# Kernel optimization log

Measured on AMD Instinct MI355X. Metric: run time of the kernel, lower is better.

The kernel has to match this reference:

```python
import jax, jax.numpy as jnp
import numpy as np

B, T, C, H = 8, 1024, 1024, 8
D = C // H  # head dim

def setup_inputs() -> dict:
    key = jax.random.key(0)
    ks = jax.random.split(key, 6)
    s = 1.0 / np.sqrt(C)
    return {
        "x": jax.random.normal(ks[0], (B, T, C), jnp.float32),
        "mask": jnp.ones((B, T), jnp.int32),
        "Wq": jax.random.normal(ks[1], (C, C), jnp.float32) * s,
        "bq": jnp.zeros((C,), jnp.float32),
        "Wk": jax.random.normal(ks[2], (C, C), jnp.float32) * s,
        "bk": jnp.zeros((C,), jnp.float32),
        "Wv": jax.random.normal(ks[3], (C, C), jnp.float32) * s,
        "bv": jnp.zeros((C,), jnp.float32),
        "Wp": jax.random.normal(ks[4], (C, C), jnp.float32) * s,
        "bp": jnp.zeros((C,), jnp.float32),
    }

def reference(x, mask, Wq, bq, Wk, bk, Wv, bv, Wp, bp):
    # torch Linear: x @ W.T + b
    q = (x @ Wq.T + bq).reshape(B, T, H, D).transpose(0, 2, 1, 3)  # b h t d
    k = (x @ Wk.T + bk).reshape(B, T, H, D).transpose(0, 2, 1, 3)
    v = (x @ Wv.T + bv).reshape(B, T, H, D).transpose(0, 2, 1, 3)
    att = jnp.einsum('bhqd,bhkd->bhqk', q, k) * (1.0 / np.sqrt(D))
    m = mask.astype(jnp.float32)[:, None, None, :]  # (B,1,1,T)
    att = jnp.where(m == 0, -jnp.inf, att)
    att = jax.nn.softmax(att, axis=-1)
    y = jnp.einsum('bhqk,bhkd->bhqd', att, v)
    y = y.transpose(0, 2, 1, 3).reshape(B, T, C)
    return y @ Wp.T + bp
```

## Files before the change

kernel.cpp:

```cpp
#include <hip/hip_runtime.h>

typedef __bf16 bf16;
typedef __attribute__((ext_vector_type(8))) bf16 bf16x8;
typedef __attribute__((ext_vector_type(4))) float f32x4;

#define GLDS16(g, l) __builtin_amdgcn_global_load_lds( \
    (const __attribute__((address_space(1))) void*)(g), \
    (__attribute__((address_space(3))) void*)(l), 16, 0, 0)

#define QSCALE 0.12751744f

static __device__ __forceinline__ f32x4 MFMA(bf16x8 a, bf16x8 b, f32x4 c) {
    return __builtin_amdgcn_mfma_f32_16x16x32_bf16(a, b, c, 0, 0, 0);
}

__global__ __launch_bounds__(256) void convert_kernel(
    const float* __restrict__ x, const float* __restrict__ wq,
    const float* __restrict__ wk, const float* __restrict__ wv,
    const float* __restrict__ wp,
    bf16* __restrict__ xb, bf16* __restrict__ wqkvb, bf16* __restrict__ wpb)
{
    int bid = blockIdx.x;
    const float* src; bf16* dst; int base;
    if (bid < 4096)      { src = x;  dst = xb;              base = bid * 2048; }
    else if (bid < 4608) { src = wq; dst = wqkvb;           base = (bid - 4096) * 2048; }
    else if (bid < 5120) { src = wk; dst = wqkvb + 1048576; base = (bid - 4608) * 2048; }
    else if (bid < 5632) { src = wv; dst = wqkvb + 2097152; base = (bid - 5120) * 2048; }
    else                 { src = wp; dst = wpb;             base = (bid - 5632) * 2048; }
    int i = base + threadIdx.x * 8;
    const f32x4* s4 = (const f32x4*)(src + i);
    f32x4 a = s4[0], c = s4[1];
    bf16x8 v;
    #pragma unroll
    for (int e = 0; e < 4; ++e) { v[e] = (bf16)a[e]; v[e + 4] = (bf16)c[e]; }
    *(bf16x8*)(dst + i) = v;
}

template <int MODE, int NTN>
__global__ __launch_bounds__(256, 2) void gemm2(
    const bf16* __restrict__ A, const bf16* __restrict__ B,
    const float* __restrict__ bias0, const float* __restrict__ bias1,
    const float* __restrict__ bias2,
    bf16* __restrict__ q_out, bf16* __restrict__ k_out, bf16* __restrict__ vt_out,
    float* __restrict__ f_out)
{
    constexpr int K = 1024;
    constexpr int NT = K / 64;
    constexpr int NWG = 64 * NTN;
    const int tid = threadIdx.x;
    const int lane = tid & 63;
    const int wid = tid >> 6;
    const int wr = wid >> 1, wc = wid & 1;
    const int l15 = lane & 15, l4 = lane >> 4, l7 = lane & 7;

    const int g = blockIdx.x;
    const int lin = (g & 7) * (NWG / 8) + (g >> 3);
    const int m0 = (lin / NTN) * 128, n0 = (lin % NTN) * 128;

    __shared__ __align__(16) bf16 lds[2][2][8192];

    const int rr = tid >> 3, pc = tid & 7;
    auto stage = [&](int buf, int t) {
        #pragma unroll
        for (int c = 0; c < 4; ++c) {
            int row = c * 32 + rr;
            int lc = pc ^ (row & 7);
            GLDS16(A + (size_t)(m0 + row) * K + t * 64 + lc * 8,
                   &lds[buf][0][c * 2048 + tid * 8]);
        }
        #pragma unroll
        for (int c = 0; c < 4; ++c) {
            int row = c * 32 + rr;
            int lc = pc ^ (row & 7);
            GLDS16(B + (size_t)(n0 + row) * K + t * 64 + lc * 8,
                   &lds[buf][1][c * 2048 + tid * 8]);
        }
    };

    const int arow = wr * 64 + l15;
    const int brow = wc * 64 + l15;
    #define RA(buf, f, kk) (*(const bf16x8*)((const char*)lds[buf][0] + \
        (arow + (f) * 16) * 128 + ((((kk) * 4 + l4) ^ l7) * 16)))
    #define RB(buf, j, kk) (*(const bf16x8*)((const char*)lds[buf][1] + \
        (brow + (j) * 16) * 128 + ((((kk) * 4 + l4) ^ l7) * 16)))

    f32x4 acc[4][4];
    #pragma unroll
    for (int f = 0; f < 4; ++f)
        #pragma unroll
        for (int j = 0; j < 4; ++j)
            #pragma unroll
            for (int e = 0; e < 4; ++e) acc[f][j][e] = 0.f;

    stage(0, 0);
    __syncthreads();

    for (int t = 0; t < NT; ++t) {
        const int buf = t & 1;
        if (t + 1 < NT) stage(buf ^ 1, t + 1);
        bf16x8 af[4][2], bfr[4][2];
        #pragma unroll
        for (int f = 0; f < 4; ++f) { af[f][0] = RA(buf, f, 0); af[f][1] = RA(buf, f, 1); }
        #pragma unroll
        for (int j = 0; j < 4; ++j) { bfr[j][0] = RB(buf, j, 0); bfr[j][1] = RB(buf, j, 1); }
        __builtin_amdgcn_s_setprio(1);
        #pragma unroll
        for (int f = 0; f < 4; ++f)
            #pragma unroll
            for (int j = 0; j < 4; ++j) {
                acc[f][j] = MFMA(af[f][0], bfr[j][0], acc[f][j]);
                acc[f][j] = MFMA(af[f][1], bfr[j][1], acc[f][j]);
            }
        __builtin_amdgcn_s_setprio(0);
        __syncthreads();
    }
    #undef RA
    #undef RB

    #pragma unroll
    for (int f = 0; f < 4; ++f) {
        #pragma unroll
        for (int j = 0; j < 4; ++j) {
            #pragma unroll
            for (int r = 0; r < 4; ++r) {
                int m = m0 + wr * 64 + f * 16 + l4 * 4 + r;
                int n = n0 + wc * 64 + j * 16 + l15;
                float v = acc[f][j][r];
                if (MODE == 0) {
                    if (n0 < 1024) {
                        q_out[m * 1024 + n] = (bf16)((v + bias0[n]) * QSCALE);
                    } else if (n0 < 2048) {
                        int nn = n - 1024;
                        k_out[m * 1024 + nn] = (bf16)(v + bias1[nn]);
                    } else {
                        int nn = n - 2048;
                        int hl = nn >> 7, d = nn & 127;
                        int bb = m >> 10, tt = m & 1023;
                        vt_out[((bb * 8 + hl) * 128 + d) * 1024 + tt] = (bf16)(v + bias2[nn]);
                    }
                } else {
                    f_out[m * 1024 + n] = v + bias0[n];
                }
            }
        }
    }
}

__global__ __launch_bounds__(256, 2) void attn_kernel(
    const bf16* __restrict__ qb, const bf16* __restrict__ kb,
    const bf16* __restrict__ vtb, const int* __restrict__ mask,
    bf16* __restrict__ yb)
{
    const int tid = threadIdx.x;
    const int lane = tid & 63;
    const int wid = tid >> 6;
    const int g = blockIdx.x;
    const int orig = (g & 7) * 64 + (g >> 3);
    const int bh = orig >> 3;
    const int qt = orig & 7;
    const int b = bh >> 3;
    const int h = bh & 7;
    const int m0 = b * 1024 + qt * 128;
    const int l15 = lane & 15, l4 = lane >> 4;

    __shared__ __align__(16) char smem[81920];

    auto stageKV = [&](int bufKV, int kt) {
        char* Kb = smem + bufKV * 16384;
        char* Vb = smem + 32768 + bufKV * 16384;
        #pragma unroll
        for (int n = 0; n < 4; ++n)
            GLDS16(kb + (b * 1024 + kt + n * 16 + (tid >> 4)) * 1024 + h * 128 +
                       (((tid & 15) ^ ((tid >> 4) & 7)) * 8),
                   Kb + n * 4096 + tid * 16);
        #pragma unroll
        for (int n = 0; n < 4; ++n)
            GLDS16(vtb + (bh * 128 + n * 32 + (tid >> 3)) * 1024 + kt +
                       (((tid & 7) ^ ((tid >> 3) & 7)) * 8),
                   Vb + n * 4096 + tid * 16);
    };

    bf16x8 qf[2][4];
    #pragma unroll
    for (int i = 0; i < 2; ++i)
        #pragma unroll
        for (int kc = 0; kc < 4; ++kc)
            qf[i][kc] = *(const bf16x8*)(qb +
                (m0 + wid * 32 + i * 16 + l15) * 1024 + h * 128 + kc * 32 + l4 * 8);

    f32x4 o[2][8];
    #pragma unroll
    for (int i = 0; i < 2; ++i)
        #pragma unroll
        for (int jd = 0; jd < 8; ++jd)
            #pragma unroll
            for (int e = 0; e < 4; ++e) o[i][jd][e] = 0.f;
    float l_run[2][4];
    #pragma unroll
    for (int i = 0; i < 2; ++i)
        #pragma unroll
        for (int r = 0; r < 4; ++r) l_run[i][r] = 0.f;

    stageKV(0, 0);
    __syncthreads();

    for (int t = 0; t < 16; ++t) {
        const int buf = t & 1;
        const int kt = t * 64;
        if (t + 1 < 16) stageKV(buf ^ 1, kt + 64);

        int mv[4];
        #pragma unroll
        for (int j = 0; j < 4; ++j)
            mv[j] = mask[b * 1024 + kt + j * 16 + l15];

        const char* Ks = smem + buf * 16384;
        const char* Vs = smem + 32768 + buf * 16384;

        f32x4 s[2][4];
        #pragma unroll
        for (int i = 0; i < 2; ++i)
            #pragma unroll
            for (int j = 0; j < 4; ++j)
                #pragma unroll
                for (int e = 0; e < 4; ++e) s[i][j][e] = 0.f;
        #pragma unroll
        for (int kc = 0; kc < 4; ++kc) {
            bf16x8 kf[4];
            #pragma unroll
            for (int j = 0; j < 4; ++j)
                kf[j] = *(const bf16x8*)(Ks + (j * 16 + l15) * 256 +
                    (((kc * 4 + l4) ^ (lane & 7)) * 16));
            __builtin_amdgcn_s_setprio(1);
            #pragma unroll
            for (int i = 0; i < 2; ++i)
                #pragma unroll
                for (int j = 0; j < 4; ++j)
                    s[i][j] = MFMA(qf[i][kc], kf[j], s[i][j]);
            __builtin_amdgcn_s_setprio(0);
        }

        #pragma unroll
        for (int i = 0; i < 2; ++i)
            #pragma unroll
            for (int j = 0; j < 4; ++j) {
                if (mv[j] == 0) {
                    #pragma unroll
                    for (int e = 0; e < 4; ++e) s[i][j][e] = -1e30f;
                }
                #pragma unroll
                for (int r = 0; r < 4; ++r) {
                    float p = __builtin_amdgcn_exp2f(s[i][j][r]);
                    s[i][j][r] = p;
                    l_run[i][r] += p;
                }
            }

        #pragma unroll
        for (int i = 0; i < 2; ++i)
            #pragma unroll
            for (int j = 0; j < 4; ++j)
                #pragma unroll
                for (int r = 0; r < 4; ++r) {
                    int row = i * 16 + l4 * 4 + r;
                    int col = j * 16 + l15;
                    *(bf16*)(smem + 65536 + wid * 4096 + row * 128 +
                             (((col >> 3) ^ (row & 7)) * 16) + (col & 7) * 2) =
                        (bf16)s[i][j][r];
                }

        #pragma unroll
        for (int k2 = 0; k2 < 2; ++k2) {
            bf16x8 pa[2];
            #pragma unroll
            for (int i = 0; i < 2; ++i)
                pa[i] = *(const bf16x8*)(smem + 65536 + wid * 4096 +
                    (i * 16 + l15) * 128 + (((k2 * 4 + l4) ^ (l15 & 7)) * 16));
            __builtin_amdgcn_s_setprio(1);
            #pragma unroll
            for (int jd = 0; jd < 8; ++jd) {
                bf16x8 vf = *(const bf16x8*)(Vs + (jd * 16 + l15) * 128 +
                    (((k2 * 4 + l4) ^ (l15 & 7)) * 16));
                o[0][jd] = MFMA(pa[0], vf, o[0][jd]);
                o[1][jd] = MFMA(pa[1], vf, o[1][jd]);
            }
            __builtin_amdgcn_s_setprio(0);
        }
        __syncthreads();
    }

    #pragma unroll
    for (int off = 8; off >= 1; off >>= 1)
        #pragma unroll
        for (int i = 0; i < 2; ++i)
            #pragma unroll
            for (int r = 0; r < 4; ++r) l_run[i][r] += __shfl_xor(l_run[i][r], off);
    #pragma unroll
    for (int i = 0; i < 2; ++i) {
        float inv[4];
        #pragma unroll
        for (int r = 0; r < 4; ++r) inv[r] = 1.0f / fmaxf(l_run[i][r], 1e-30f);
        #pragma unroll
        for (int jd = 0; jd < 8; ++jd)
            #pragma unroll
            for (int r = 0; r < 4; ++r)
                yb[(m0 + wid * 32 + i * 16 + l4 * 4 + r) * 1024 +
                   h * 128 + jd * 16 + l15] = (bf16)(o[i][jd][r] * inv[r]);
    }
}

extern "C" void kernel_launch(void* const* d_in, const int* in_sizes, int n_in,
                              void* d_out, int out_size, void* d_ws, size_t ws_size,
                              hipStream_t stream)
{
    (void)in_sizes; (void)n_in; (void)out_size; (void)ws_size;
    const float* x  = (const float*)d_in[0];
    const int* mask = (const int*)d_in[1];
    const float* Wq = (const float*)d_in[2];
    const float* bq = (const float*)d_in[3];
    const float* Wk = (const float*)d_in[4];
    const float* bk = (const float*)d_in[5];
    const float* Wv = (const float*)d_in[6];
    const float* bv = (const float*)d_in[7];
    const float* Wp = (const float*)d_in[8];
    const float* bp = (const float*)d_in[9];
    float* out = (float*)d_out;

    char* ws = (char*)d_ws;
    bf16* xb    = (bf16*)(ws);
    bf16* wqkvb = (bf16*)(ws + (16u << 20));
    bf16* wpb   = (bf16*)(ws + (22u << 20));
    bf16* qbuf  = (bf16*)(ws + (24u << 20));
    bf16* kbuf  = (bf16*)(ws + (40u << 20));
    bf16* vtb   = (bf16*)(ws + (56u << 20));
    bf16* ybuf  = (bf16*)(ws + (72u << 20));

    convert_kernel<<<6144, 256, 0, stream>>>(x, Wq, Wk, Wv, Wp, xb, wqkvb, wpb);
    gemm2<0, 24><<<1536, 256, 0, stream>>>(xb, wqkvb, bq, bk, bv,
                                           qbuf, kbuf, vtb, nullptr);
    attn_kernel<<<512, 256, 0, stream>>>(qbuf, kbuf, vtb, mask, ybuf);
    gemm2<1, 8><<<512, 256, 0, stream>>>(ybuf, wpb, bp, nullptr, nullptr,
                                         nullptr, nullptr, nullptr, out);
}
```

Before: 172.7 us.

## Replace LDS-staged GEMM with direct global-to-register MFMA operand loads

The projection GEMMs drop LDS double-buffering and barriers. Each wave now loads its MFMA A/B fragments straight from global memory into registers, with a two-deep register prefetch, and the occupancy hint is raised to 3 blocks per CU. This removes LDS traffic and __syncthreads stalls. The cost is that operands are no longer shared across waves, so global and L2 traffic roughly doubles, and the per-lane loads are strided 16-byte rows that coalesce poorly.

```diff
diff --git a/kernel.cpp b/kernel.cpp
--- a/kernel.cpp
+++ b/kernel.cpp
@@ -37,7 +37,7 @@
 }
 
 template <int MODE, int NTN>
-__global__ __launch_bounds__(256, 2) void gemm2(
+__global__ __launch_bounds__(256, 3) void gemmd(
     const bf16* __restrict__ A, const bf16* __restrict__ B,
     const float* __restrict__ bias0, const float* __restrict__ bias1,
     const float* __restrict__ bias2,
@@ -45,77 +45,58 @@
     float* __restrict__ f_out)
 {
     constexpr int K = 1024;
-    constexpr int NT = K / 64;
     constexpr int NWG = 64 * NTN;
     const int tid = threadIdx.x;
     const int lane = tid & 63;
     const int wid = tid >> 6;
     const int wr = wid >> 1, wc = wid & 1;
-    const int l15 = lane & 15, l4 = lane >> 4, l7 = lane & 7;
+    const int l15 = lane & 15, l4 = lane >> 4;
 
     const int g = blockIdx.x;
     const int lin = (g & 7) * (NWG / 8) + (g >> 3);
     const int m0 = (lin / NTN) * 128, n0 = (lin % NTN) * 128;
 
-    __shared__ __align__(16) bf16 lds[2][2][8192];
-
-    const int rr = tid >> 3, pc = tid & 7;
-    auto stage = [&](int buf, int t) {
-        #pragma unroll
-        for (int c = 0; c < 4; ++c) {
-            int row = c * 32 + rr;
-            int lc = pc ^ (row & 7);
-            GLDS16(A + (size_t)(m0 + row) * K + t * 64 + lc * 8,
-                   &lds[buf][0][c * 2048 + tid * 8]);
+    const bf16* pA = A + (size_t)(m0 + wr * 64 + l15) * K + l4 * 8;
+    const bf16* pB = B + (size_t)(n0 + wc * 64 + l15) * K + l4 * 8;
+    #define LA(f, t) (*(const bf16x8*)(pA + (size_t)(f) * 16 * K + (t) * 32))
+    #define LB(j, t) (*(const bf16x8*)(pB + (size_t)(j) * 16 * K + (t) * 32))
+
+    f32x4 acc[4][4];
+    #pragma unroll
+    for (int f = 0; f < 4; ++f)
+        #pragma unroll
+        for (int j = 0; j < 4; ++j)
+            #pragma unroll
+            for (int e = 0; e < 4; ++e) acc[f][j][e] = 0.f;
+
+    bf16x8 a0[4], b0[4], a1[4], b1[4];
+    #pragma unroll
+    for (int f = 0; f < 4; ++f) { a0[f] = LA(f, 0); b0[f] = LB(f, 0); }
+
+    for (int t = 0; t < 32; t += 2) {
+        #pragma unroll
+        for (int f = 0; f < 4; ++f) { a1[f] = LA(f, t + 1); b1[f] = LB(f, t + 1); }
+        __builtin_amdgcn_s_setprio(1);
+        #pragma unroll
+        for (int f = 0; f < 4; ++f)
+            #pragma unroll
+            for (int j = 0; j < 4; ++j)
+                acc[f][j] = MFMA(a0[f], b0[j], acc[f][j]);
+        __builtin_amdgcn_s_setprio(0);
+        if (t + 2 < 32) {
+            #pragma unroll
+            for (int f = 0; f < 4; ++f) { a0[f] = LA(f, t + 2); b0[f] = LB(f, t + 2); }
         }
-        #pragma unroll
-        for (int c = 0; c < 4; ++c) {
-            int row = c * 32 + rr;
-            int lc = pc ^ (row & 7);
-            GLDS16(B + (size_t)(n0 + row) * K + t * 64 + lc * 8,
-                   &lds[buf][1][c * 2048 + tid * 8]);
-        }
-    };
-
-    const int arow = wr * 64 + l15;
-    const int brow = wc * 64 + l15;
-    #define RA(buf, f, kk) (*(const bf16x8*)((const char*)lds[buf][0] + \
-        (arow + (f) * 16) * 128 + ((((kk) * 4 + l4) ^ l7) * 16)))
-    #define RB(buf, j, kk) (*(const bf16x8*)((const char*)lds[buf][1] + \
-        (brow + (j) * 16) * 128 + ((((kk) * 4 + l4) ^ l7) * 16)))
-
-    f32x4 acc[4][4];
-    #pragma unroll
-    for (int f = 0; f < 4; ++f)
-        #pragma unroll
-        for (int j = 0; j < 4; ++j)
-            #pragma unroll
-            for (int e = 0; e < 4; ++e) acc[f][j][e] = 0.f;
-
-    stage(0, 0);
-    __syncthreads();
-
-    for (int t = 0; t < NT; ++t) {
-        const int buf = t & 1;
-        if (t + 1 < NT) stage(buf ^ 1, t + 1);
-        bf16x8 af[4][2], bfr[4][2];
-        #pragma unroll
-        for (int f = 0; f < 4; ++f) { af[f][0] = RA(buf, f, 0); af[f][1] = RA(buf, f, 1); }
-        #pragma unroll
-        for (int j = 0; j < 4; ++j) { bfr[j][0] = RB(buf, j, 0); bfr[j][1] = RB(buf, j, 1); }
         __builtin_amdgcn_s_setprio(1);
         #pragma unroll
         for (int f = 0; f < 4; ++f)
             #pragma unroll
-            for (int j = 0; j < 4; ++j) {
-                acc[f][j] = MFMA(af[f][0], bfr[j][0], acc[f][j]);
-                acc[f][j] = MFMA(af[f][1], bfr[j][1], acc[f][j]);
-            }
+            for (int j = 0; j < 4; ++j)
+                acc[f][j] = MFMA(a1[f], b1[j], acc[f][j]);
         __builtin_amdgcn_s_setprio(0);
-        __syncthreads();
     }
-    #undef RA
-    #undef RB
+    #undef LA
+    #undef LB
 
     #pragma unroll
     for (int f = 0; f < 4; ++f) {
@@ -164,7 +145,6 @@
     const int l15 = lane & 15, l4 = lane >> 4;
 
     __shared__ __align__(16) char smem[81920];
-
     auto stageKV = [&](int bufKV, int kt) {
         char* Kb = smem + bufKV * 16384;
         char* Vb = smem + 32768 + bufKV * 16384;
@@ -336,9 +316,9 @@
     bf16* ybuf  = (bf16*)(ws + (72u << 20));
 
     convert_kernel<<<6144, 256, 0, stream>>>(x, Wq, Wk, Wv, Wp, xb, wqkvb, wpb);
-    gemm2<0, 24><<<1536, 256, 0, stream>>>(xb, wqkvb, bq, bk, bv,
+    gemmd<0, 24><<<1536, 256, 0, stream>>>(xb, wqkvb, bq, bk, bv,
                                            qbuf, kbuf, vtb, nullptr);
     attn_kernel<<<512, 256, 0, stream>>>(qbuf, kbuf, vtb, mask, ybuf);
-    gemm2<1, 8><<<512, 256, 0, stream>>>(ybuf, wpb, bp, nullptr, nullptr,
+    gemmd<1, 8><<<512, 256, 0, stream>>>(ybuf, wpb, bp, nullptr, nullptr,
                                          nullptr, nullptr, nullptr, out);
 }
```

New measurement: 316.9 us. 1.84x slower.

## Restructure GEMM to two waves with 64x128 warp tiles and K-step 32

Applied to the files above, without the earlier changes.

The projection GEMM now runs with 128 threads (two waves) per block instead of four. Each wave computes a 64x128 output slab, and the K tile per stage shrinks from 64 to 32 with a new XOR-swizzled LDS layout that packs two rows per 128-byte line. The aim is more register-level reuse of LDS fragments per MFMA and half the shared memory per block. In exchange it doubles the number of K iterations and barriers, holds 128 accumulator floats per lane, and halves the waves available to hide latency.

```diff
diff --git a/kernel.cpp b/kernel.cpp
--- a/kernel.cpp
+++ b/kernel.cpp
@@ -37,7 +37,7 @@
 }
 
 template <int MODE, int NTN>
-__global__ __launch_bounds__(256, 2) void gemm2(
+__global__ __launch_bounds__(128, 2) void gemm2(
     const bf16* __restrict__ A, const bf16* __restrict__ B,
     const float* __restrict__ bias0, const float* __restrict__ bias1,
     const float* __restrict__ bias2,
@@ -45,50 +45,44 @@
     float* __restrict__ f_out)
 {
     constexpr int K = 1024;
-    constexpr int NT = K / 64;
+    constexpr int NT = K / 32;
     constexpr int NWG = 64 * NTN;
     const int tid = threadIdx.x;
     const int lane = tid & 63;
     const int wid = tid >> 6;
-    const int wr = wid >> 1, wc = wid & 1;
-    const int l15 = lane & 15, l4 = lane >> 4, l7 = lane & 7;
+    const int l15 = lane & 15, l4 = lane >> 4;
 
     const int g = blockIdx.x;
     const int lin = (g & 7) * (NWG / 8) + (g >> 3);
     const int m0 = (lin / NTN) * 128, n0 = (lin % NTN) * 128;
 
-    __shared__ __align__(16) bf16 lds[2][2][8192];
-
-    const int rr = tid >> 3, pc = tid & 7;
+    __shared__ __align__(16) bf16 lds[2][2][4096];
+
+    const int qq = (tid & 7) ^ ((tid >> 3) & 7);
+    const int rb = 2 * (tid >> 3) + (qq >> 2);
+    const int cc = qq & 3;
+    const bf16* aB = A + (size_t)(m0 + rb) * K + cc * 8;
+    const bf16* bB = B + (size_t)(n0 + rb) * K + cc * 8;
     auto stage = [&](int buf, int t) {
         #pragma unroll
-        for (int c = 0; c < 4; ++c) {
-            int row = c * 32 + rr;
-            int lc = pc ^ (row & 7);
-            GLDS16(A + (size_t)(m0 + row) * K + t * 64 + lc * 8,
-                   &lds[buf][0][c * 2048 + tid * 8]);
-        }
-        #pragma unroll
-        for (int c = 0; c < 4; ++c) {
-            int row = c * 32 + rr;
-            int lc = pc ^ (row & 7);
-            GLDS16(B + (size_t)(n0 + row) * K + t * 64 + lc * 8,
-                   &lds[buf][1][c * 2048 + tid * 8]);
-        }
+        for (int c = 0; c < 4; ++c)
+            GLDS16(aB + (size_t)(c * 32) * K + t * 32, &lds[buf][0][c * 1024 + tid * 8]);
+        #pragma unroll
+        for (int c = 0; c < 4; ++c)
+            GLDS16(bB + (size_t)(c * 32) * K + t * 32, &lds[buf][1][c * 1024 + tid * 8]);
     };
 
-    const int arow = wr * 64 + l15;
-    const int brow = wc * 64 + l15;
-    #define RA(buf, f, kk) (*(const bf16x8*)((const char*)lds[buf][0] + \
-        (arow + (f) * 16) * 128 + ((((kk) * 4 + l4) ^ l7) * 16)))
-    #define RB(buf, j, kk) (*(const bf16x8*)((const char*)lds[buf][1] + \
-        (brow + (j) * 16) * 128 + ((((kk) * 4 + l4) ^ l7) * 16)))
-
-    f32x4 acc[4][4];
+    const int physc = (((l15 & 1) * 4 + l4) ^ ((l15 >> 1) & 7)) * 16;
+    const int aoff = (wid * 32 + (l15 >> 1)) * 128 + physc;
+    const int boff = (l15 >> 1) * 128 + physc;
+    #define RA(buf, f) (*(const bf16x8*)((const char*)lds[buf][0] + aoff + (f) * 1024))
+    #define RB(buf, j) (*(const bf16x8*)((const char*)lds[buf][1] + boff + (j) * 1024))
+
+    f32x4 acc[4][8];
     #pragma unroll
     for (int f = 0; f < 4; ++f)
         #pragma unroll
-        for (int j = 0; j < 4; ++j)
+        for (int j = 0; j < 8; ++j)
             #pragma unroll
             for (int e = 0; e < 4; ++e) acc[f][j][e] = 0.f;
 
@@ -98,19 +92,17 @@
     for (int t = 0; t < NT; ++t) {
         const int buf = t & 1;
         if (t + 1 < NT) stage(buf ^ 1, t + 1);
-        bf16x8 af[4][2], bfr[4][2];
-        #pragma unroll
-        for (int f = 0; f < 4; ++f) { af[f][0] = RA(buf, f, 0); af[f][1] = RA(buf, f, 1); }
-        #pragma unroll
-        for (int j = 0; j < 4; ++j) { bfr[j][0] = RB(buf, j, 0); bfr[j][1] = RB(buf, j, 1); }
+        bf16x8 af[4], bfr[8];
+        #pragma unroll
+        for (int f = 0; f < 4; ++f) af[f] = RA(buf, f);
+        #pragma unroll
+        for (int j = 0; j < 8; ++j) bfr[j] = RB(buf, j);
         __builtin_amdgcn_s_setprio(1);
         #pragma unroll
         for (int f = 0; f < 4; ++f)
             #pragma unroll
-            for (int j = 0; j < 4; ++j) {
-                acc[f][j] = MFMA(af[f][0], bfr[j][0], acc[f][j]);
-                acc[f][j] = MFMA(af[f][1], bfr[j][1], acc[f][j]);
-            }
+            for (int j = 0; j < 8; ++j)
+                acc[f][j] = MFMA(af[f], bfr[j], acc[f][j]);
         __builtin_amdgcn_s_setprio(0);
         __syncthreads();
     }
@@ -120,11 +112,11 @@
     #pragma unroll
     for (int f = 0; f < 4; ++f) {
         #pragma unroll
-        for (int j = 0; j < 4; ++j) {
+        for (int j = 0; j < 8; ++j) {
             #pragma unroll
             for (int r = 0; r < 4; ++r) {
-                int m = m0 + wr * 64 + f * 16 + l4 * 4 + r;
-                int n = n0 + wc * 64 + j * 16 + l15;
+                int m = m0 + wid * 64 + f * 16 + l4 * 4 + r;
+                int n = n0 + j * 16 + l15;
                 float v = acc[f][j][r];
                 if (MODE == 0) {
                     if (n0 < 1024) {
@@ -164,7 +156,6 @@
     const int l15 = lane & 15, l4 = lane >> 4;
 
     __shared__ __align__(16) char smem[81920];
-
     auto stageKV = [&](int bufKV, int kt) {
         char* Kb = smem + bufKV * 16384;
         char* Vb = smem + 32768 + bufKV * 16384;
@@ -336,9 +327,9 @@
     bf16* ybuf  = (bf16*)(ws + (72u << 20));
 
     convert_kernel<<<6144, 256, 0, stream>>>(x, Wq, Wk, Wv, Wp, xb, wqkvb, wpb);
-    gemm2<0, 24><<<1536, 256, 0, stream>>>(xb, wqkvb, bq, bk, bv,
+    gemm2<0, 24><<<1536, 128, 0, stream>>>(xb, wqkvb, bq, bk, bv,
                                            qbuf, kbuf, vtb, nullptr);
     attn_kernel<<<512, 256, 0, stream>>>(qbuf, kbuf, vtb, mask, ybuf);
-    gemm2<1, 8><<<512, 256, 0, stream>>>(ybuf, wpb, bp, nullptr, nullptr,
+    gemm2<1, 8><<<512, 128, 0, stream>>>(ybuf, wpb, bp, nullptr, nullptr,
                                          nullptr, nullptr, nullptr, out);
 }
```

Result: slower. 191.8 us (+11.1%).

## Use 256x256-tile 8-wave ping-pong GEMM for fused QKV projection

Applied to the files above, without the earlier changes.

Replaces the 128x128-tile, 4-wave QKV projection GEMM with a 256x256-tile, 512-thread kernel. Its finely phased schedule interleaves LDS fragment reads, global-to-LDS prefetch and MFMA bursts, using explicit barriers, waitcnt and priority hints. Larger tiles raise arithmetic intensity per loaded byte and the phasing overlaps memory with compute. The cost is more register pressure from a 32-accumulator tile, only 384 workgroups (fewer waves to fill CUs), and heavier LDS use. The output projection GEMM is only cleaned up to a non-templated mode.

```diff
diff --git a/kernel.cpp b/kernel.cpp
--- a/kernel.cpp
+++ b/kernel.cpp
@@ -36,13 +36,213 @@
     *(bf16x8*)(dst + i) = v;
 }
 
-template <int MODE, int NTN>
-__global__ __launch_bounds__(256, 2) void gemm2(
+template <int NTN>
+__global__ __launch_bounds__(512, 2) void gemm8p(
     const bf16* __restrict__ A, const bf16* __restrict__ B,
     const float* __restrict__ bias0, const float* __restrict__ bias1,
     const float* __restrict__ bias2,
-    bf16* __restrict__ q_out, bf16* __restrict__ k_out, bf16* __restrict__ vt_out,
-    float* __restrict__ f_out)
+    bf16* __restrict__ q_out, bf16* __restrict__ k_out, bf16* __restrict__ vt_out)
+{
+    constexpr int K = 1024;
+    constexpr int NWG = 32 * NTN;
+    const int tid = threadIdx.x;
+    const int lane = tid & 63;
+    const int wid = tid >> 6;
+    const int wr = wid >> 2;
+    const int wc = wid & 3;
+    const int l15 = lane & 15, l4 = lane >> 4, l7 = lane & 7;
+
+    const int g = blockIdx.x;
+    const int lin = (g & 7) * (NWG / 8) + (g >> 3);
+    const int m0 = (lin / NTN) * 256, n0 = (lin % NTN) * 256;
+
+    __shared__ __align__(16) bf16 lds[2][2][16384];
+
+    const int srow = tid >> 3;
+    const int lc = (tid & 7) ^ (srow & 7);
+    auto stageIdx = [&](int idx) {
+        const int t = idx >> 2;
+        const int buf = t & 1;
+        const int mm = (idx >> 1) & 1;
+        const int h = idx & 1;
+        const bf16* src = (mm ? B + (size_t)(n0 + h * 128 + srow) * K
+                              : A + (size_t)(m0 + h * 128 + srow) * K) + t * 64 + lc * 8;
+        bf16* dst = &lds[buf][mm][h * 8192 + tid * 8];
+        GLDS16(src, dst);
+        GLDS16(src + (size_t)64 * K, dst + 4096);
+    };
+
+    #define RA8(buf, f, kk) (*(const bf16x8*)((const char*)lds[buf][0] + \
+        (wr * 128 + (f) * 16 + l15) * 128 + ((((kk) * 4 + l4) ^ l7) * 16)))
+    #define RB8(buf, j, kk) (*(const bf16x8*)((const char*)lds[buf][1] + \
+        (wc * 64 + (j) * 16 + l15) * 128 + ((((kk) * 4 + l4) ^ l7) * 16)))
+
+    f32x4 acc[8][4];
+    #pragma unroll
+    for (int f = 0; f < 8; ++f)
+        #pragma unroll
+        for (int j = 0; j < 4; ++j)
+            #pragma unroll
+            for (int e = 0; e < 4; ++e) acc[f][j][e] = 0.f;
+
+    stageIdx(0); stageIdx(1); stageIdx(2); stageIdx(3); stageIdx(4);
+    asm volatile("s_waitcnt vmcnt(2)" ::: "memory");
+    __builtin_amdgcn_sched_barrier(0);
+    __builtin_amdgcn_s_barrier();
+    __builtin_amdgcn_sched_barrier(0);
+
+    bf16x8 af[4][2], bfr[4][2];
+
+    #define PH_TOP() \
+        __builtin_amdgcn_s_barrier(); \
+        asm volatile("s_waitcnt lgkmcnt(0)" ::: "memory"); \
+        __builtin_amdgcn_sched_barrier(0); \
+        __builtin_amdgcn_s_setprio(1)
+    #define PH_BOT() \
+        __builtin_amdgcn_s_setprio(0)
+    #define PH_END() \
+        __builtin_amdgcn_s_barrier(); \
+        __builtin_amdgcn_sched_barrier(0)
+
+    for (int i = 0; i < 8; ++i) {
+        const int s = 8 * i;
+        #pragma unroll
+        for (int f = 0; f < 4; ++f) { af[f][0] = RA8(0, f, 0); af[f][1] = RA8(0, f, 1); }
+        #pragma unroll
+        for (int j = 0; j < 2; ++j) { bfr[j][0] = RB8(0, j, 0); bfr[j][1] = RB8(0, j, 1); }
+        if (s + 5 < 64) stageIdx(s + 5);
+        PH_TOP();
+        #pragma unroll
+        for (int f = 0; f < 4; ++f)
+            #pragma unroll
+            for (int j = 0; j < 2; ++j) {
+                acc[f][j] = MFMA(af[f][0], bfr[j][0], acc[f][j]);
+                acc[f][j] = MFMA(af[f][1], bfr[j][1], acc[f][j]);
+            }
+        PH_BOT(); PH_END();
+        #pragma unroll
+        for (int j = 2; j < 4; ++j) { bfr[j][0] = RB8(0, j, 0); bfr[j][1] = RB8(0, j, 1); }
+        if (s + 6 < 64) stageIdx(s + 6);
+        PH_TOP();
+        #pragma unroll
+        for (int f = 0; f < 4; ++f)
+            #pragma unroll
+            for (int j = 2; j < 4; ++j) {
+                acc[f][j] = MFMA(af[f][0], bfr[j][0], acc[f][j]);
+                acc[f][j] = MFMA(af[f][1], bfr[j][1], acc[f][j]);
+            }
+        PH_BOT(); PH_END();
+        #pragma unroll
+        for (int f = 0; f < 4; ++f) { af[f][0] = RA8(0, f + 4, 0); af[f][1] = RA8(0, f + 4, 1); }
+        if (s + 7 < 64) stageIdx(s + 7);
+        PH_TOP();
+        #pragma unroll
+        for (int f = 0; f < 4; ++f)
+            #pragma unroll
+            for (int j = 2; j < 4; ++j) {
+                acc[f + 4][j] = MFMA(af[f][0], bfr[j][0], acc[f + 4][j]);
+                acc[f + 4][j] = MFMA(af[f][1], bfr[j][1], acc[f + 4][j]);
+            }
+        PH_BOT(); PH_END();
+        if (s + 8 < 64) stageIdx(s + 8);
+        PH_TOP();
+        #pragma unroll
+        for (int f = 0; f < 4; ++f)
+            #pragma unroll
+            for (int j = 0; j < 2; ++j) {
+                acc[f + 4][j] = MFMA(af[f][0], bfr[j][0], acc[f + 4][j]);
+                acc[f + 4][j] = MFMA(af[f][1], bfr[j][1], acc[f + 4][j]);
+            }
+        PH_BOT();
+        if (i < 7) asm volatile("s_waitcnt vmcnt(2)" ::: "memory");
+        else       asm volatile("s_waitcnt vmcnt(0)" ::: "memory");
+        PH_END();
+        #pragma unroll
+        for (int f = 0; f < 4; ++f) { af[f][0] = RA8(1, f, 0); af[f][1] = RA8(1, f, 1); }
+        #pragma unroll
+        for (int j = 0; j < 2; ++j) { bfr[j][0] = RB8(1, j, 0); bfr[j][1] = RB8(1, j, 1); }
+        if (s + 9 < 64) stageIdx(s + 9);
+        PH_TOP();
+        #pragma unroll
+        for (int f = 0; f < 4; ++f)
+            #pragma unroll
+            for (int j = 0; j < 2; ++j) {
+                acc[f][j] = MFMA(af[f][0], bfr[j][0], acc[f][j]);
+                acc[f][j] = MFMA(af[f][1], bfr[j][1], acc[f][j]);
+            }
+        PH_BOT(); PH_END();
+        #pragma unroll
+        for (int j = 2; j < 4; ++j) { bfr[j][0] = RB8(1, j, 0); bfr[j][1] = RB8(1, j, 1); }
+        if (s + 10 < 64) stageIdx(s + 10);
+        PH_TOP();
+        #pragma unroll
+        for (int f = 0; f < 4; ++f)
+            #pragma unroll
+            for (int j = 2; j < 4; ++j) {
+                acc[f][j] = MFMA(af[f][0], bfr[j][0], acc[f][j]);
+                acc[f][j] = MFMA(af[f][1], bfr[j][1], acc[f][j]);
+            }
+        PH_BOT(); PH_END();
+        #pragma unroll
+        for (int f = 0; f < 4; ++f) { af[f][0] = RA8(1, f + 4, 0); af[f][1] = RA8(1, f + 4, 1); }
+        if (s + 11 < 64) stageIdx(s + 11);
+        PH_TOP();
+        #pragma unroll
+        for (int f = 0; f < 4; ++f)
+            #pragma unroll
+            for (int j = 2; j < 4; ++j) {
+                acc[f + 4][j] = MFMA(af[f][0], bfr[j][0], acc[f + 4][j]);
+                acc[f + 4][j] = MFMA(af[f][1], bfr[j][1], acc[f + 4][j]);
+            }
+        PH_BOT(); PH_END();
+        if (s + 12 < 64) stageIdx(s + 12);
+        PH_TOP();
+        #pragma unroll
+        for (int f = 0; f < 4; ++f)
+            #pragma unroll
+            for (int j = 0; j < 2; ++j) {
+                acc[f + 4][j] = MFMA(af[f][0], bfr[j][0], acc[f + 4][j]);
+                acc[f + 4][j] = MFMA(af[f][1], bfr[j][1], acc[f + 4][j]);
+            }
+        PH_BOT();
+        if (i < 7) asm volatile("s_waitcnt vmcnt(2)" ::: "memory");
+        PH_END();
+    }
+    #undef RA8
+    #undef RB8
+    #undef PH_TOP
+    #undef PH_BOT
+    #undef PH_END
+
+    #pragma unroll
+    for (int f = 0; f < 8; ++f) {
+        #pragma unroll
+        for (int j = 0; j < 4; ++j) {
+            #pragma unroll
+            for (int r = 0; r < 4; ++r) {
+                int m = m0 + wr * 128 + f * 16 + l4 * 4 + r;
+                int n = n0 + wc * 64 + j * 16 + l15;
+                float v = acc[f][j][r];
+                if (n0 < 1024) {
+                    q_out[m * 1024 + n] = (bf16)((v + bias0[n]) * QSCALE);
+                } else if (n0 < 2048) {
+                    int nn = n - 1024;
+                    k_out[m * 1024 + nn] = (bf16)(v + bias1[nn]);
+                } else {
+                    int nn = n - 2048;
+                    int hl = nn >> 7, d = nn & 127;
+                    int bb = m >> 10, tt = m & 1023;
+                    vt_out[((bb * 8 + hl) * 128 + d) * 1024 + tt] = (bf16)(v + bias2[nn]);
+                }
+            }
+        }
+    }
+}
+
+template <int NTN>
+__global__ __launch_bounds__(256, 2) void gemm2(
+    const bf16* __restrict__ A, const bf16* __restrict__ B,
+    const float* __restrict__ bias0, float* __restrict__ f_out)
 {
     constexpr int K = 1024;
     constexpr int NT = K / 64;
@@ -118,32 +318,15 @@
     #undef RB
 
     #pragma unroll
-    for (int f = 0; f < 4; ++f) {
-        #pragma unroll
-        for (int j = 0; j < 4; ++j) {
+    for (int f = 0; f < 4; ++f)
+        #pragma unroll
+        for (int j = 0; j < 4; ++j)
             #pragma unroll
             for (int r = 0; r < 4; ++r) {
                 int m = m0 + wr * 64 + f * 16 + l4 * 4 + r;
                 int n = n0 + wc * 64 + j * 16 + l15;
-                float v = acc[f][j][r];
-                if (MODE == 0) {
-                    if (n0 < 1024) {
-                        q_out[m * 1024 + n] = (bf16)((v + bias0[n]) * QSCALE);
-                    } else if (n0 < 2048) {
-                        int nn = n - 1024;
-                        k_out[m * 1024 + nn] = (bf16)(v + bias1[nn]);
-                    } else {
-                        int nn = n - 2048;
-                        int hl = nn >> 7, d = nn & 127;
-                        int bb = m >> 10, tt = m & 1023;
-                        vt_out[((bb * 8 + hl) * 128 + d) * 1024 + tt] = (bf16)(v + bias2[nn]);
-                    }
-                } else {
-                    f_out[m * 1024 + n] = v + bias0[n];
-                }
-            }
-        }
-    }
+                f_out[m * 1024 + n] = acc[f][j][r] + bias0[n];
+            }
 }
 
 __global__ __launch_bounds__(256, 2) void attn_kernel(
@@ -164,7 +347,6 @@
     const int l15 = lane & 15, l4 = lane >> 4;
 
     __shared__ __align__(16) char smem[81920];
-
     auto stageKV = [&](int bufKV, int kt) {
         char* Kb = smem + bufKV * 16384;
         char* Vb = smem + 32768 + bufKV * 16384;
@@ -336,9 +518,7 @@
     bf16* ybuf  = (bf16*)(ws + (72u << 20));
 
     convert_kernel<<<6144, 256, 0, stream>>>(x, Wq, Wk, Wv, Wp, xb, wqkvb, wpb);
-    gemm2<0, 24><<<1536, 256, 0, stream>>>(xb, wqkvb, bq, bk, bv,
-                                           qbuf, kbuf, vtb, nullptr);
+    gemm8p<12><<<384, 512, 0, stream>>>(xb, wqkvb, bq, bk, bv, qbuf, kbuf, vtb);
     attn_kernel<<<512, 256, 0, stream>>>(qbuf, kbuf, vtb, mask, ybuf);
-    gemm2<1, 8><<<512, 256, 0, stream>>>(ybuf, wpb, bp, nullptr, nullptr,
-                                         nullptr, nullptr, nullptr, out);
+    gemm2<8><<<512, 256, 0, stream>>>(ybuf, wpb, bp, out);
 }
```

After: 181.6 us. 5.2% more time.
